# Performance work log

Hardware: AMD Instinct MI355X
Metric: run time of the kernel (lower is better)

Reference implementation:

```python
import jax, jax.numpy as jnp
import numpy as np

B, N, H = 8192, 8, 256
EDGE_DIM = 16
HALF = EDGE_DIM // 2  # 8: emb half + scalar half
THR = 0.4
PAIR_OFFS = [(0, N), (0, 2 * N), (N, 2 * N)]  # (text,audio), (text,facial), (audio,facial)
E_PER = 6 * (N - 1) + 6 * N  # 90 edges per sample


def _base_edge_index():
    # Static per-sample topology (matches the torch loop ordering exactly).
    src, dst = [], []
    for m in range(3):  # temporal edges, both directions interleaved
        for i in range(N - 1):
            u, v = m * N + i, m * N + i + 1
            src += [u, v]; dst += [v, u]
    for oa, ob in PAIR_OFFS:  # cross-modal edges
        for i in range(N):
            src += [oa + i, ob + i]; dst += [ob + i, oa + i]
    return np.array([src, dst], dtype=np.int64)  # (2, E_PER)

_BASE_EI = _base_edge_index()


def _l2norm(x):
    return x / jnp.maximum(jnp.linalg.norm(x, axis=-1, keepdims=True), 1e-12)


def setup_inputs() -> dict:
    key = jax.random.key(0)
    ks = jax.random.split(key, 6)
    s = 1.0 / np.sqrt(H)
    return {
        "z_text_segs": jax.random.normal(ks[0], (B, N, H), jnp.float32),
        "z_audio_segs": jax.random.normal(ks[1], (B, N, H), jnp.float32),
        "z_facial_segs": jax.random.normal(ks[2], (B, N, H), jnp.float32),
        "Wq": jax.random.normal(ks[3], (H // 2, H), jnp.float32) * s,
        "bq": jnp.zeros((H // 2,), jnp.float32),
        "Wk": jax.random.normal(ks[4], (H // 2, H), jnp.float32) * s,
        "bk": jnp.zeros((H // 2,), jnp.float32),
        "emb": jax.random.normal(ks[5], (5, HALF), jnp.float32),
    }


def reference(z_text_segs, z_audio_segs, z_facial_segs, Wq, bq, Wk, bk, emb):
    nodes = jnp.concatenate([z_text_segs, z_audio_segs, z_facial_segs], axis=1)  # (B, 3N, H)
    q = _l2norm(nodes @ Wq.T + bq)  # (B, 3N, H/2)
    k = _l2norm(nodes @ Wk.T + bk)

    # Cross-modal discrepancy, pair-major then segment (matches loop order): P = 3N
    a_idx = np.concatenate([oa + np.arange(N) for oa, _ in PAIR_OFFS])
    b_idx = np.concatenate([ob + np.arange(N) for _, ob in PAIR_OFFS])
    disc = 1.0 - jax.nn.sigmoid(jnp.einsum('bph,bph->bp', q[:, a_idx], k[:, b_idx]))  # (B, P)

    etype = jnp.where(disc > THR, 4, 3)  # (B, P) int
    z = jnp.zeros_like(disc)
    # scalar half: [disc_w, temp_dist, direction, etype/4, pad...]
    cross_scal = jnp.stack([disc, z, z, etype.astype(jnp.float32) / 4.0] + [z] * (HALF - 4), axis=-1)
    cross_attr = jnp.concatenate([emb[etype], cross_scal], axis=-1)  # (B, P, EDGE_DIM)
    cross_attr = jnp.repeat(cross_attr, 2, axis=1)  # both directions share the attr

    # Temporal edge attrs: constant per modality m in {0,1,2}
    mz = jnp.zeros((3,), jnp.float32)
    t_scal = jnp.stack([mz, jnp.full((3,), 1.0 / N), jnp.ones((3,)),
                        jnp.arange(3, dtype=jnp.float32) / 4.0] + [mz] * (HALF - 4), axis=-1)
    t_attr = jnp.concatenate([emb[:3], t_scal], axis=-1)  # (3, EDGE_DIM)
    t_attr = jnp.repeat(t_attr, 2 * (N - 1), axis=0)  # (6(N-1), EDGE_DIM)
    t_attr = jnp.broadcast_to(t_attr, (B,) + t_attr.shape)

    edge_attr = jnp.concatenate([t_attr, cross_attr], axis=1).reshape(B * E_PER, EDGE_DIM)

    ei = _BASE_EI[:, None, :] + (np.arange(B, dtype=np.int64) * 3 * N)[None, :, None]
    edge_index = jnp.asarray(ei.reshape(2, B * E_PER))

    node_feats = nodes.reshape(B * 3 * N, H)
    batch_vec = jnp.repeat(jnp.arange(B), 3 * N)
    return node_feats, edge_index, edge_attr, batch_vec
```

## Files before the change

kernel.cpp:

```cpp
#include <hip/hip_runtime.h>

#define BB 8192
#define NSEG 8
#define HH 256
#define HO 128
#define NODES 24
#define EPER 90
#define NF_SIZE (BB * NODES * HH)
#define EI_OFF  NF_SIZE
#define EI_SIZE (2 * BB * EPER)
#define EA_OFF  (EI_OFF + EI_SIZE)
#define EA_SIZE (BB * EPER * 16)
#define BV_OFF  (EA_OFF + EA_SIZE)

__global__ __launch_bounds__(256) void transpose_w(
    const float4* __restrict__ Wq4, const float4* __restrict__ Wk4,
    float4* __restrict__ ws)
{
    int idx = blockIdx.x * 256 + threadIdx.x;
    const float4* src = (idx < 8192) ? Wq4 : Wk4;
    int j  = idx & 8191;
    int o  = j >> 6;
    int kk = j & 63;
    float4 v = src[j];
    ws[(idx & 8192) + kk * 128 + o] = v;
}

template <bool TW>
__global__ __launch_bounds__(256) void htdg_kernel(
    const float* __restrict__ zt, const float* __restrict__ za,
    const float* __restrict__ zf,
    const float* __restrict__ Wq, const float* __restrict__ bq,
    const float* __restrict__ Wk, const float* __restrict__ bk,
    const float* __restrict__ emb, const float4* __restrict__ wt,
    float* __restrict__ out)
{
    __shared__ float xs[NODES * HH];
    __shared__ float uv[32 * HO];
    __shared__ float nrm_part[32 * 8];
    __shared__ float dot_part[24 * 8];
    __shared__ float rnorm_s[32];
    __shared__ float disc_s[24];
    __shared__ int   et_s[24];
    __shared__ float emb_s[40];

    const int b   = blockIdx.x;
    const int tid = threadIdx.x;

    {
        float4*       xs4 = (float4*)xs;
        float4*       nf  = (float4*)out + (size_t)b * 1536;
        #pragma unroll
        for (int it = 0; it < 6; ++it) {
            int j = tid + it * 256;
            int m = j >> 9;
            int w = j & 511;
            const float4* sp = (m == 0 ? (const float4*)zt
                               : m == 1 ? (const float4*)za
                                        : (const float4*)zf) + (size_t)b * 512 + w;
            float4 v = *sp;
            xs4[j] = v;
            nf[j]  = v;
        }
        if (tid < 40) emb_s[tid] = emb[tid];
    }

    {
        int j = tid;
        if (j < 180) {
            int d = (j >= 90) ? 1 : 0;
            int e = j - d * 90;
            int s, dd;
            if (e < 42) {
                int m = e / 14;
                int r = e - m * 14;
                int i = r >> 1;
                int u = m * 8 + i;
                if (r & 1) { s = u + 1; dd = u; } else { s = u; dd = u + 1; }
            } else {
                int p  = (e - 42) >> 1;
                int pr = p >> 3;
                int i  = p & 7;
                int a  = (pr == 2 ? 8 : 0) + i;
                int bb = (pr == 0 ? 8 : 16) + i;
                if (e & 1) { s = bb; dd = a; } else { s = a; dd = bb; }
            }
            int val = ((d == 0) ? s : dd) + b * 24;
            out[(size_t)EI_OFF + (size_t)d * (BB * EPER) + (size_t)b * EPER + e] = (float)val;
        }
        if (tid < 24) out[(size_t)BV_OFF + (size_t)b * 24 + tid] = (float)b;
    }
    __syncthreads();

    {
        const int wave = tid >> 6;
        const int lane = tid & 63;
        const float* bias;  int nodeBase, slotBase;
        if (wave < 2) { bias = bq; nodeBase = wave * 8;           slotBase = wave * 8; }
        else          { bias = bk; nodeBase = (wave - 2) * 8 + 8; slotBase = wave * 8; }

        const float4* Wt = TW ? (wt + ((wave < 2) ? 0 : 8192)) : nullptr;
        const float*  Wb  = (wave < 2) ? Wq : Wk;
        const float4* Wr0 = (const float4*)Wb + (size_t)lane * 64;
        const float4* Wr1 = (const float4*)Wb + (size_t)(lane + 64) * 64;

        const float4* xb  = (const float4*)xs + nodeBase * 64;

        float acc0[8] = {0,0,0,0,0,0,0,0};
        float acc1[8] = {0,0,0,0,0,0,0,0};
        for (int kk = 0; kk < 64; ++kk) {
            float4 w0, w1;
            if (TW) {
                w0 = Wt[kk * 128 + lane];
                w1 = Wt[kk * 128 + 64 + lane];
            } else {
                w0 = Wr0[kk];
                w1 = Wr1[kk];
            }
            #pragma unroll
            for (int n = 0; n < 8; ++n) {
                float4 xv = xb[n * 64 + kk];
                acc0[n] += w0.x * xv.x + w0.y * xv.y + w0.z * xv.z + w0.w * xv.w;
                acc1[n] += w1.x * xv.x + w1.y * xv.y + w1.z * xv.z + w1.w * xv.w;
            }
        }
        float b0 = bias[lane], b1 = bias[lane + 64];
        #pragma unroll
        for (int n = 0; n < 8; ++n) {
            uv[(slotBase + n) * HO + lane]      = acc0[n] + b0;
            uv[(slotBase + n) * HO + 64 + lane] = acc1[n] + b1;
        }
    }
    __syncthreads();

    {
        int slot = tid >> 3, part = tid & 7;
        const float* u = &uv[slot * HO + part * 16];
        float s = 0.f;
        #pragma unroll
        for (int o = 0; o < 16; ++o) { float v = u[o]; s += v * v; }
        nrm_part[tid] = s;
    }
    if (tid < 192) {
        int p = tid >> 3, part = tid & 7;
        int pr = p >> 3, i = p & 7;
        int aslot = (pr == 2 ? 8 : 0) + i;
        int bslot = (pr == 0 ? 16 : 24) + i;
        const float* ua = &uv[aslot * HO + part * 16];
        const float* vb = &uv[bslot * HO + part * 16];
        float s = 0.f;
        #pragma unroll
        for (int o = 0; o < 16; ++o) s += ua[o] * vb[o];
        dot_part[tid] = s;
    }
    __syncthreads();
    if (tid < 32) {
        float s = 0.f;
        #pragma unroll
        for (int j = 0; j < 8; ++j) s += nrm_part[tid * 8 + j];
        rnorm_s[tid] = 1.0f / fmaxf(sqrtf(s), 1e-12f);
    }
    __syncthreads();
    if (tid < 24) {
        float s = 0.f;
        #pragma unroll
        for (int j = 0; j < 8; ++j) s += dot_part[tid * 8 + j];
        int pr = tid >> 3, i = tid & 7;
        int aslot = (pr == 2 ? 8 : 0) + i;
        int bslot = (pr == 0 ? 16 : 24) + i;
        float t   = s * rnorm_s[aslot] * rnorm_s[bslot];
        float dsc = 1.0f / (1.0f + expf(t));
        disc_s[tid] = dsc;
        et_s[tid]   = (dsc > 0.4f) ? 4 : 3;
    }
    __syncthreads();

    {
        float* ea = out + (size_t)EA_OFF + (size_t)b * (EPER * 16);
        #pragma unroll
        for (int it = 0; it < 6; ++it) {
            int j = tid + it * 256;
            if (j < 1440) {
                int row = j >> 4, c = j & 15;
                float val;
                if (row < 42) {
                    int m = row / 14;
                    if      (c < 8)   val = emb_s[m * 8 + c];
                    else if (c == 9)  val = 0.125f;
                    else if (c == 10) val = 1.0f;
                    else if (c == 11) val = (float)m * 0.25f;
                    else              val = 0.0f;
                } else {
                    int p  = (row - 42) >> 1;
                    int et = et_s[p];
                    if      (c < 8)   val = emb_s[et * 8 + c];
                    else if (c == 8)  val = disc_s[p];
                    else if (c == 11) val = (float)et * 0.25f;
                    else              val = 0.0f;
                }
                ea[j] = val;
            }
        }
    }
}

extern "C" void kernel_launch(void* const* d_in, const int* in_sizes, int n_in,
                              void* d_out, int out_size, void* d_ws, size_t ws_size,
                              hipStream_t stream) {
    const float* zt  = (const float*)d_in[0];
    const float* za  = (const float*)d_in[1];
    const float* zf  = (const float*)d_in[2];
    const float* Wq  = (const float*)d_in[3];
    const float* bq  = (const float*)d_in[4];
    const float* Wk  = (const float*)d_in[5];
    const float* bk  = (const float*)d_in[6];
    const float* emb = (const float*)d_in[7];

    if (d_ws && ws_size >= (size_t)2 * 8192 * sizeof(float4)) {
        float4* ws = (float4*)d_ws;
        transpose_w<<<64, 256, 0, stream>>>((const float4*)Wq, (const float4*)Wk, ws);
        htdg_kernel<true><<<BB, 256, 0, stream>>>(zt, za, zf, Wq, bq, Wk, bk, emb,
                                                  ws, (float*)d_out);
    } else {
        htdg_kernel<false><<<BB, 256, 0, stream>>>(zt, za, zf, Wq, bq, Wk, bk, emb,
                                                   nullptr, (float*)d_out);
    }
}
```

Baseline: 640.6 us.

## Process two samples per block and stream node features via scalar loads

Each block now handles two batch samples, so every transposed weight float4 loaded per lane is reused across 16 nodes instead of 8. The node features are no longer staged in LDS. They are read straight from global memory with inline s_load_dwordx4 scalar loads, double-buffered between the two samples with explicit lgkmcnt waits, and the next weight row is prefetched. This removes the LDS round-trip for the input and halves weight traffic per sample, at the cost of heavier register pressure, half as many blocks, and fragile inline asm. The fallback path for a missing workspace is also dropped.

New measurement: 659.6 us. 1.03x slower.

```diff
diff --git a/kernel.cpp b/kernel.cpp
--- a/kernel.cpp
+++ b/kernel.cpp
@@ -1,7 +1,7 @@
 #include <hip/hip_runtime.h>
+#include <stdint.h>
 
 #define BB 8192
-#define NSEG 8
 #define HH 256
 #define HO 128
 #define NODES 24
@@ -12,6 +12,36 @@
 #define EA_OFF  (EI_OFF + EI_SIZE)
 #define EA_SIZE (BB * EPER * 16)
 #define BV_OFF  (EA_OFF + EA_SIZE)
+
+typedef float f4 __attribute__((ext_vector_type(4)));
+
+#define SL(dst, base, IMM) \
+    asm volatile("s_load_dwordx4 %0, %1, " IMM : "=s"(dst) : "s"(base))
+
+#define SWAIT8(a0,a1,a2,a3,a4,a5,a6,a7) \
+    asm volatile("s_waitcnt lgkmcnt(0)" \
+                 : "+s"(a0),"+s"(a1),"+s"(a2),"+s"(a3), \
+                   "+s"(a4),"+s"(a5),"+s"(a6),"+s"(a7))
+
+#define FMA4(acc, W_, X_) \
+    acc = fmaf((W_)[0],(X_)[0],acc); acc = fmaf((W_)[1],(X_)[1],acc); \
+    acc = fmaf((W_)[2],(X_)[2],acc); acc = fmaf((W_)[3],(X_)[3],acc);
+
+#define LD8(BUF, ADDR) \
+    SL(BUF##0, ADDR, "0x0");    SL(BUF##1, ADDR, "0x400"); \
+    SL(BUF##2, ADDR, "0x800");  SL(BUF##3, ADDR, "0xc00"); \
+    SL(BUF##4, ADDR, "0x1000"); SL(BUF##5, ADDR, "0x1400"); \
+    SL(BUF##6, ADDR, "0x1800"); SL(BUF##7, ADDR, "0x1c00");
+
+#define C8(ACC0, ACC1, BUF) \
+    FMA4(ACC0[0], w0, BUF##0) FMA4(ACC1[0], w1, BUF##0) \
+    FMA4(ACC0[1], w0, BUF##1) FMA4(ACC1[1], w1, BUF##1) \
+    FMA4(ACC0[2], w0, BUF##2) FMA4(ACC1[2], w1, BUF##2) \
+    FMA4(ACC0[3], w0, BUF##3) FMA4(ACC1[3], w1, BUF##3) \
+    FMA4(ACC0[4], w0, BUF##4) FMA4(ACC1[4], w1, BUF##4) \
+    FMA4(ACC0[5], w0, BUF##5) FMA4(ACC1[5], w1, BUF##5) \
+    FMA4(ACC0[6], w0, BUF##6) FMA4(ACC1[6], w1, BUF##6) \
+    FMA4(ACC0[7], w0, BUF##7) FMA4(ACC1[7], w1, BUF##7)
 
 __global__ __launch_bounds__(256) void transpose_w(
     const float4* __restrict__ Wq4, const float4* __restrict__ Wk4,
@@ -26,157 +56,178 @@
     ws[(idx & 8192) + kk * 128 + o] = v;
 }
 
-template <bool TW>
 __global__ __launch_bounds__(256) void htdg_kernel(
     const float* __restrict__ zt, const float* __restrict__ za,
     const float* __restrict__ zf,
-    const float* __restrict__ Wq, const float* __restrict__ bq,
-    const float* __restrict__ Wk, const float* __restrict__ bk,
-    const float* __restrict__ emb, const float4* __restrict__ wt,
+    const float* __restrict__ bq, const float* __restrict__ bk,
+    const float* __restrict__ emb, const float* __restrict__ wt,
     float* __restrict__ out)
 {
-    __shared__ float xs[NODES * HH];
-    __shared__ float uv[32 * HO];
-    __shared__ float nrm_part[32 * 8];
-    __shared__ float dot_part[24 * 8];
-    __shared__ float rnorm_s[32];
-    __shared__ float disc_s[24];
-    __shared__ int   et_s[24];
+    __shared__ float uv[2 * 32 * HO];
+    __shared__ float nrm_part[2][256];
+    __shared__ float dot_part[2][192];
+    __shared__ float rnorm_s[2][32];
+    __shared__ float disc_s[2][24];
+    __shared__ int   et_s[2][24];
     __shared__ float emb_s[40];
 
-    const int b   = blockIdx.x;
+    const int b0  = blockIdx.x * 2;
     const int tid = threadIdx.x;
 
     {
-        float4*       xs4 = (float4*)xs;
-        float4*       nf  = (float4*)out + (size_t)b * 1536;
-        #pragma unroll
-        for (int it = 0; it < 6; ++it) {
+        const f4* zt4 = (const f4*)zt + (size_t)b0 * 512;
+        const f4* za4 = (const f4*)za + (size_t)b0 * 512;
+        const f4* zf4 = (const f4*)zf + (size_t)b0 * 512;
+        f4* nf = (f4*)out + (size_t)b0 * 1536;
+        #pragma unroll
+        for (int it = 0; it < 12; ++it) {
             int j = tid + it * 256;
-            int m = j >> 9;
-            int w = j & 511;
-            const float4* sp = (m == 0 ? (const float4*)zt
-                               : m == 1 ? (const float4*)za
-                                        : (const float4*)zf) + (size_t)b * 512 + w;
-            float4 v = *sp;
-            xs4[j] = v;
-            nf[j]  = v;
+            int s = (it >= 6);
+            int rem = j - s * 1536;
+            int m = rem >> 9, w = rem & 511;
+            const f4* sp = (m == 0 ? zt4 : m == 1 ? za4 : zf4) + s * 512 + w;
+            nf[j] = *sp;
         }
         if (tid < 40) emb_s[tid] = emb[tid];
     }
 
-    {
+    #pragma unroll
+    for (int s = 0; s < 2; ++s) {
+        int b = b0 + s;
         int j = tid;
         if (j < 180) {
             int d = (j >= 90) ? 1 : 0;
             int e = j - d * 90;
-            int s, dd;
+            int ss, dd;
             if (e < 42) {
                 int m = e / 14;
                 int r = e - m * 14;
                 int i = r >> 1;
                 int u = m * 8 + i;
-                if (r & 1) { s = u + 1; dd = u; } else { s = u; dd = u + 1; }
+                if (r & 1) { ss = u + 1; dd = u; } else { ss = u; dd = u + 1; }
             } else {
                 int p  = (e - 42) >> 1;
                 int pr = p >> 3;
                 int i  = p & 7;
                 int a  = (pr == 2 ? 8 : 0) + i;
                 int bb = (pr == 0 ? 8 : 16) + i;
-                if (e & 1) { s = bb; dd = a; } else { s = a; dd = bb; }
+                if (e & 1) { ss = bb; dd = a; } else { ss = a; dd = bb; }
             }
-            int val = ((d == 0) ? s : dd) + b * 24;
+            int val = ((d == 0) ? ss : dd) + b * 24;
             out[(size_t)EI_OFF + (size_t)d * (BB * EPER) + (size_t)b * EPER + e] = (float)val;
         }
         if (tid < 24) out[(size_t)BV_OFF + (size_t)b * 24 + tid] = (float)b;
     }
-    __syncthreads();
 
     {
         const int wave = tid >> 6;
         const int lane = tid & 63;
-        const float* bias;  int nodeBase, slotBase;
-        if (wave < 2) { bias = bq; nodeBase = wave * 8;           slotBase = wave * 8; }
-        else          { bias = bk; nodeBase = (wave - 2) * 8 + 8; slotBase = wave * 8; }
-
-        const float4* Wt = TW ? (wt + ((wave < 2) ? 0 : 8192)) : nullptr;
-        const float*  Wb  = (wave < 2) ? Wq : Wk;
-        const float4* Wr0 = (const float4*)Wb + (size_t)lane * 64;
-        const float4* Wr1 = (const float4*)Wb + (size_t)(lane + 64) * 64;
-
-        const float4* xb  = (const float4*)xs + nodeBase * 64;
-
-        float acc0[8] = {0,0,0,0,0,0,0,0};
-        float acc1[8] = {0,0,0,0,0,0,0,0};
+        const f4* Wt4 = (const f4*)wt + ((wave < 2) ? 0 : 8192);
+        const float* zsel = (wave == 0) ? zt : (wave == 3) ? zf : za;
+        const float* bias = (wave < 2) ? bq : bk;
+        const int slotBase = wave * 8;
+
+        uint64_t xb;
+        {
+            uint64_t v = (uint64_t)zsel + (uint64_t)b0 * 8192;
+            uint32_t lo = __builtin_amdgcn_readfirstlane((uint32_t)v);
+            uint32_t hi = __builtin_amdgcn_readfirstlane((uint32_t)(v >> 32));
+            xb = ((uint64_t)hi << 32) | lo;
+        }
+
+        float A0r0[8] = {0,0,0,0,0,0,0,0}, A0r1[8] = {0,0,0,0,0,0,0,0};
+        float A1r0[8] = {0,0,0,0,0,0,0,0}, A1r1[8] = {0,0,0,0,0,0,0,0};
+        f4 x0, x1, x2, x3, x4, x5, x6, x7;
+        f4 y0, y1, y2, y3, y4, y5, y6, y7;
+
+        f4 w0 = Wt4[lane];
+        f4 w1 = Wt4[64 + lane];
+
+        LD8(x, xb);
+
         for (int kk = 0; kk < 64; ++kk) {
-            float4 w0, w1;
-            if (TW) {
-                w0 = Wt[kk * 128 + lane];
-                w1 = Wt[kk * 128 + 64 + lane];
-            } else {
-                w0 = Wr0[kk];
-                w1 = Wr1[kk];
-            }
+            int kn = (kk < 63) ? kk + 1 : 63;
+            f4 nw0 = Wt4[kn * 128 + lane];
+            f4 nw1 = Wt4[kn * 128 + 64 + lane];
+            uint64_t aB = xb + (uint64_t)(8192 + kk * 16);
+            uint64_t aA = xb + (uint64_t)(kn * 16);
+
+            SWAIT8(x0, x1, x2, x3, x4, x5, x6, x7);
+            LD8(y, aB);
+            C8(A0r0, A0r1, x);
+
+            SWAIT8(y0, y1, y2, y3, y4, y5, y6, y7);
+            LD8(x, aA);
+            C8(A1r0, A1r1, y);
+
+            w0 = nw0; w1 = nw1;
+        }
+        asm volatile("s_waitcnt lgkmcnt(0)");
+
+        float bb0 = bias[lane], bb1 = bias[lane + 64];
+        #pragma unroll
+        for (int n = 0; n < 8; ++n) {
+            uv[(slotBase + n) * HO + lane]             = A0r0[n] + bb0;
+            uv[(slotBase + n) * HO + 64 + lane]        = A0r1[n] + bb1;
+            uv[4096 + (slotBase + n) * HO + lane]      = A1r0[n] + bb0;
+            uv[4096 + (slotBase + n) * HO + 64 + lane] = A1r1[n] + bb1;
+        }
+    }
+    __syncthreads();
+
+    #pragma unroll
+    for (int s = 0; s < 2; ++s) {
+        const float* uvS = uv + s * 4096;
+        {
+            int slot = tid >> 3, part = tid & 7;
+            const float* u = &uvS[slot * HO + part * 16];
+            float sum = 0.f;
             #pragma unroll
-            for (int n = 0; n < 8; ++n) {
-                float4 xv = xb[n * 64 + kk];
-                acc0[n] += w0.x * xv.x + w0.y * xv.y + w0.z * xv.z + w0.w * xv.w;
-                acc1[n] += w1.x * xv.x + w1.y * xv.y + w1.z * xv.z + w1.w * xv.w;
-            }
-        }
-        float b0 = bias[lane], b1 = bias[lane + 64];
-        #pragma unroll
-        for (int n = 0; n < 8; ++n) {
-            uv[(slotBase + n) * HO + lane]      = acc0[n] + b0;
-            uv[(slotBase + n) * HO + 64 + lane] = acc1[n] + b1;
-        }
-    }
-    __syncthreads();
-
-    {
-        int slot = tid >> 3, part = tid & 7;
-        const float* u = &uv[slot * HO + part * 16];
-        float s = 0.f;
-        #pragma unroll
-        for (int o = 0; o < 16; ++o) { float v = u[o]; s += v * v; }
-        nrm_part[tid] = s;
-    }
-    if (tid < 192) {
-        int p = tid >> 3, part = tid & 7;
-        int pr = p >> 3, i = p & 7;
-        int aslot = (pr == 2 ? 8 : 0) + i;
-        int bslot = (pr == 0 ? 16 : 24) + i;
-        const float* ua = &uv[aslot * HO + part * 16];
-        const float* vb = &uv[bslot * HO + part * 16];
-        float s = 0.f;
-        #pragma unroll
-        for (int o = 0; o < 16; ++o) s += ua[o] * vb[o];
-        dot_part[tid] = s;
-    }
-    __syncthreads();
-    if (tid < 32) {
-        float s = 0.f;
-        #pragma unroll
-        for (int j = 0; j < 8; ++j) s += nrm_part[tid * 8 + j];
-        rnorm_s[tid] = 1.0f / fmaxf(sqrtf(s), 1e-12f);
-    }
-    __syncthreads();
-    if (tid < 24) {
-        float s = 0.f;
-        #pragma unroll
-        for (int j = 0; j < 8; ++j) s += dot_part[tid * 8 + j];
-        int pr = tid >> 3, i = tid & 7;
-        int aslot = (pr == 2 ? 8 : 0) + i;
-        int bslot = (pr == 0 ? 16 : 24) + i;
-        float t   = s * rnorm_s[aslot] * rnorm_s[bslot];
-        float dsc = 1.0f / (1.0f + expf(t));
-        disc_s[tid] = dsc;
-        et_s[tid]   = (dsc > 0.4f) ? 4 : 3;
-    }
-    __syncthreads();
-
-    {
-        float* ea = out + (size_t)EA_OFF + (size_t)b * (EPER * 16);
+            for (int o = 0; o < 16; ++o) { float v = u[o]; sum += v * v; }
+            nrm_part[s][tid] = sum;
+        }
+        if (tid < 192) {
+            int p = tid >> 3, part = tid & 7;
+            int pr = p >> 3, i = p & 7;
+            int aslot = (pr == 2 ? 8 : 0) + i;
+            int bslot = (pr == 0 ? 16 : 24) + i;
+            const float* ua = &uvS[aslot * HO + part * 16];
+            const float* vb = &uvS[bslot * HO + part * 16];
+            float sum = 0.f;
+            #pragma unroll
+            for (int o = 0; o < 16; ++o) sum += ua[o] * vb[o];
+            dot_part[s][tid] = sum;
+        }
+    }
+    __syncthreads();
+    if (tid < 64) {
+        int s = tid >> 5, sl = tid & 31;
+        float sum = 0.f;
+        #pragma unroll
+        for (int j = 0; j < 8; ++j) sum += nrm_part[s][sl * 8 + j];
+        rnorm_s[s][sl] = 1.0f / fmaxf(sqrtf(sum), 1e-12f);
+    }
+    __syncthreads();
+    if (tid < 64) {
+        int s = tid >> 5, p = tid & 31;
+        if (p < 24) {
+            float sum = 0.f;
+            #pragma unroll
+            for (int j = 0; j < 8; ++j) sum += dot_part[s][p * 8 + j];
+            int pr = p >> 3, i = p & 7;
+            int aslot = (pr == 2 ? 8 : 0) + i;
+            int bslot = (pr == 0 ? 16 : 24) + i;
+            float t   = sum * rnorm_s[s][aslot] * rnorm_s[s][bslot];
+            float dsc = 1.0f / (1.0f + expf(t));
+            disc_s[s][p] = dsc;
+            et_s[s][p]   = (dsc > 0.4f) ? 4 : 3;
+        }
+    }
+    __syncthreads();
+
+    #pragma unroll
+    for (int s = 0; s < 2; ++s) {
+        float* ea = out + (size_t)EA_OFF + (size_t)(b0 + s) * (EPER * 16);
         #pragma unroll
         for (int it = 0; it < 6; ++it) {
             int j = tid + it * 256;
@@ -192,9 +243,9 @@
                     else              val = 0.0f;
                 } else {
                     int p  = (row - 42) >> 1;
-                    int et = et_s[p];
+                    int et = et_s[s][p];
                     if      (c < 8)   val = emb_s[et * 8 + c];
-                    else if (c == 8)  val = disc_s[p];
+                    else if (c == 8)  val = disc_s[s][p];
                     else if (c == 11) val = (float)et * 0.25f;
                     else              val = 0.0f;
                 }
@@ -216,13 +267,8 @@
     const float* bk  = (const float*)d_in[6];
     const float* emb = (const float*)d_in[7];
 
-    if (d_ws && ws_size >= (size_t)2 * 8192 * sizeof(float4)) {
-        float4* ws = (float4*)d_ws;
-        transpose_w<<<64, 256, 0, stream>>>((const float4*)Wq, (const float4*)Wk, ws);
-        htdg_kernel<true><<<BB, 256, 0, stream>>>(zt, za, zf, Wq, bq, Wk, bk, emb,
-                                                  ws, (float*)d_out);
-    } else {
-        htdg_kernel<false><<<BB, 256, 0, stream>>>(zt, za, zf, Wq, bq, Wk, bk, emb,
-                                                   nullptr, (float*)d_out);
-    }
+    float4* ws = (float4*)d_ws;
+    transpose_w<<<64, 256, 0, stream>>>((const float4*)Wq, (const float4*)Wk, ws);
+    htdg_kernel<<<BB / 2, 256, 0, stream>>>(zt, za, zf, bq, bk, emb,
+                                            (const float*)ws, (float*)d_out);
 }
```
